# Kernel optimization log

Hardware: AMD Instinct MI355X
Metric: run time of the kernel (lower is better)

Reference implementation:

```python
import jax, jax.numpy as jnp
import numpy as np

N_NODES = 100000
N_HIGH = 20000
N_EDGES = 200000
D = 128
HEADS = 4
EPS = 1e-16


def setup_inputs() -> dict:
    key = jax.random.key(0)
    ks = jax.random.split(key, 9)
    s = 1.0 / np.sqrt(D)
    return {
        "n_features": jax.random.normal(ks[0], (N_NODES, D), jnp.float32),
        "W_src": jax.random.normal(ks[1], (D, HEADS * D), jnp.float32) * s,
        "W_dst": jax.random.normal(ks[2], (D, HEADS * D), jnp.float32) * s,
        "att_src": jax.random.normal(ks[3], (1, HEADS, D), jnp.float32) * s,
        "att_dst": jax.random.normal(ks[4], (1, HEADS, D), jnp.float32) * s,
        "W_high": jax.random.normal(ks[5], (D, D), jnp.float32) * s,
        "b_high": jnp.zeros((D,), jnp.float32),
        "src_idx": jax.random.randint(ks[6], (N_EDGES,), 0, N_NODES),
        "dst_idx": jax.random.randint(ks[7], (N_EDGES,), 0, N_HIGH),
    }


def reference(n_features, W_src, W_dst, att_src, att_dst, W_high, b_high, src_idx, dst_idx):
    # --- edge-wise gather of node features ---
    nn_features = n_features[src_idx]                      # [E, D]
    # --- scatter-mean to hyperedge features, gather back per edge ---
    seg_sum = jax.ops.segment_sum(nn_features, dst_idx, num_segments=N_HIGH)
    cnt = jax.ops.segment_sum(jnp.ones((src_idx.shape[0],), nn_features.dtype), dst_idx, num_segments=N_HIGH)
    h_mean = seg_sum / jnp.maximum(cnt, 1.0)[:, None]       # [H, D]
    h_high_e = h_mean[dst_idx]                              # [E, D]
    # --- per-edge multi-head projections ---
    E = src_idx.shape[0]
    h_node = (nn_features @ W_src).reshape(E, HEADS, D)     # [E, h, D]
    h_high = (h_high_e @ W_dst).reshape(E, HEADS, D)        # [E, h, D]
    # --- attention scores ---
    alpha_src = (h_high * att_src).sum(-1)                  # [E, h]
    alpha_dst = (h_node * att_dst).sum(-1)                  # [E, h]
    alpha = jax.nn.leaky_relu(alpha_src + alpha_dst, 0.2)
    # --- segment softmax over edges grouped by hyperedge id ---
    amax = jax.ops.segment_max(alpha, dst_idx, num_segments=N_HIGH)
    alpha = jnp.exp(alpha - amax[dst_idx])
    asum = jax.ops.segment_sum(alpha, dst_idx, num_segments=N_HIGH)
    alpha = alpha / (asum[dst_idx] + EPS)                   # [E, h]
    # --- weight, head-mean, scatter-sum aggregate ---
    h_node = (h_node * alpha[..., None]).mean(axis=1)       # [E, D]
    h_features = jax.ops.segment_sum(h_node, dst_idx, num_segments=N_HIGH)
    h_features = h_features @ W_high + b_high               # [H, D]
    return (h_features, alpha)
```

## Files before the change

### kernel.cpp

```cpp
#include <hip/hip_runtime.h>
#include <math.h>

#define N_NODES 100000
#define N_HIGH  20000
#define N_EDGES 200000
#define D       128
#define HEADS   4
#define EPSF    1e-16f

typedef __attribute__((ext_vector_type(8))) short bf16x8;
typedef __attribute__((ext_vector_type(4))) float f32x4;
typedef unsigned short ushort_t;
typedef unsigned int uint_t;

__device__ __forceinline__ ushort_t bf16_rn(float f) {
  uint_t u = __float_as_uint(f);
  u = u + 0x7FFFu + ((u >> 16) & 1u);
  return (ushort_t)(u >> 16);
}
__device__ __forceinline__ uint_t pack_bf2(float x, float y) {
  return (uint_t)bf16_rn(x) | ((uint_t)bf16_rn(y) << 16);
}
__device__ __forceinline__ float readlane_f(float v, int q) {
  return __uint_as_float(__builtin_amdgcn_readlane(__float_as_uint(v), q));
}

constexpr size_t OFF_VSRC = 0;
constexpr size_t OFF_VDST = OFF_VSRC + 512 * 4;
constexpr size_t OFF_P    = OFF_VDST + 512 * 4;
constexpr size_t OFF_APK  = OFF_P    + 65536 * 4;
constexpr size_t OFF_CNT  = OFF_APK  + 800000 * 4;
constexpr size_t OFF_OFFS = OFF_CNT  + 20000 * 4;
constexpr size_t OFF_FILL = OFF_OFFS + 20004 * 4;
constexpr size_t OFF_SORT = OFF_FILL + 20000 * 4;
constexpr size_t OFF_G    = OFF_SORT + 200000 * 8;
constexpr size_t OFF_NFB  = OFF_G    + 20000 * 512 * 2;

__global__ __launch_bounds__(256) void k_vp(
    const float* __restrict__ Wsrc, const float* __restrict__ Wdst,
    const float* __restrict__ att_src, const float* __restrict__ att_dst,
    const float* __restrict__ Whigh,
    float* __restrict__ v_src, float* __restrict__ v_dst,
    int* __restrict__ cnt, ushort_t* __restrict__ Pt) {
  __shared__ float red[128];
  if (blockIdx.x < 256) {
    int gid = blockIdx.x * 256 + threadIdx.x;
    if (gid < N_HIGH) cnt[gid] = 0;

    int W = blockIdx.x * 4 + (threadIdx.x >> 6);
    int lane = threadIdx.x & 63;
    int which = W >> 9;
    int idx = W & 511;
    int k = idx >> 2, h = idx & 3;
    const float* wrow = (which ? Wdst : Wsrc) + k * (HEADS * D) + h * D;
    const float* arow = (which ? att_src : att_dst) + h * D;
    float2 wv = ((const float2*)wrow)[lane];
    float2 av = ((const float2*)arow)[lane];
    float s = wv.x * av.x + wv.y * av.y;
#pragma unroll
    for (int o = 32; o; o >>= 1) s += __shfl_xor(s, o);
    if (lane == 0) {
      if (which) v_src[k * HEADS + h] = s;
      else       v_dst[k * HEADS + h] = s;
    }
  } else {
    int hk = blockIdx.x - 256;
    int h = hk >> 7, col = hk & 127;
    int d = threadIdx.x & 127, half = threadIdx.x >> 7;
    const float* ws = Wsrc + col * (HEADS * D) + h * D + half * 64;
    const float* wh = Whigh + (size_t)(half * 64) * D + d;
    float s = 0.f;
#pragma unroll 8
    for (int m = 0; m < 64; ++m) s += ws[m] * wh[(size_t)m * D];
    if (half) red[d] = s;
    __syncthreads();
    if (!half) {
      int kp = (col >> 1) * 8 + h * 2 + (col & 1);
      Pt[(size_t)d * 512 + kp] = bf16_rn(0.25f * (s + red[d]));
    }
  }
}

#define NP_BLOCKS 1563
#define H_BLOCKS  782
__global__ __launch_bounds__(256) void k_nodehist(
    const float* __restrict__ nf,
    const float* __restrict__ v_src, const float* __restrict__ v_dst,
    float4* __restrict__ a_pack,
    const int* __restrict__ dst, int* __restrict__ cnt,
    ushort_t* __restrict__ nfb) {
  __shared__ float nfT[128 * 65];
  __shared__ float4 vsf4[128];
  __shared__ float4 vdf4[128];
  __shared__ float part[8][4][64];
  int t = threadIdx.x;
  if (blockIdx.x >= NP_BLOCKS) {
    int e = (blockIdx.x - NP_BLOCKS) * 256 + t;
    if (e < N_EDGES) atomicAdd(&cnt[dst[e]], 1);
    return;
  }
  int n0 = blockIdx.x * 64;

  if (t < 128) vsf4[t] = ((const float4*)v_src)[t];
  else vdf4[t - 128] = ((const float4*)v_dst)[t - 128];

  const float4* nf4 = (const float4*)nf;
#pragma unroll
  for (int j = 0; j < 8; ++j) {
    int f4 = j * 256 + t;
    int r = f4 >> 5, c4 = f4 & 31;
    int n = n0 + r;
    if (n > N_NODES - 1) n = N_NODES - 1;
    float4 g = nf4[(size_t)n * 32 + c4];
    nfT[(c4 * 4 + 0) * 65 + r] = g.x;
    nfT[(c4 * 4 + 1) * 65 + r] = g.y;
    nfT[(c4 * 4 + 2) * 65 + r] = g.z;
    nfT[(c4 * 4 + 3) * 65 + r] = g.w;
    ushort4 hb;
    hb.x = bf16_rn(g.x); hb.y = bf16_rn(g.y);
    hb.z = bf16_rn(g.z); hb.w = bf16_rn(g.w);
    ((ushort4*)nfb)[(size_t)n * 32 + c4] = hb;
  }
  __syncthreads();

  int l = t & 63, w = t >> 6;
  float as[4] = {0.f, 0.f, 0.f, 0.f};
  float ad[4] = {0.f, 0.f, 0.f, 0.f};
#pragma unroll 8
  for (int kk = 0; kk < 32; ++kk) {
    int k = w * 32 + kk;
    float x = nfT[k * 65 + l];
    float4 s4 = vsf4[k];
    float4 d4 = vdf4[k];
    as[0] += x * s4.x; as[1] += x * s4.y; as[2] += x * s4.z; as[3] += x * s4.w;
    ad[0] += x * d4.x; ad[1] += x * d4.y; ad[2] += x * d4.z; ad[3] += x * d4.w;
  }
#pragma unroll
  for (int v = 0; v < 4; ++v) {
    part[v][w][l] = as[v];
    part[v + 4][w][l] = ad[v];
  }
  __syncthreads();

  if (t < 64) {
    int ll = t;
    if (n0 + ll < N_NODES) {
      float4 o;
      o.x = part[0][0][ll] + part[0][1][ll] + part[0][2][ll] + part[0][3][ll];
      o.y = part[1][0][ll] + part[1][1][ll] + part[1][2][ll] + part[1][3][ll];
      o.z = part[2][0][ll] + part[2][1][ll] + part[2][2][ll] + part[2][3][ll];
      o.w = part[3][0][ll] + part[3][1][ll] + part[3][2][ll] + part[3][3][ll];
      a_pack[(size_t)(n0 + ll) * 2] = o;
    }
  } else if (t < 128) {
    int ll = t - 64;
    if (n0 + ll < N_NODES) {
      float4 o;
      o.x = part[4][0][ll] + part[4][1][ll] + part[4][2][ll] + part[4][3][ll];
      o.y = part[5][0][ll] + part[5][1][ll] + part[5][2][ll] + part[5][3][ll];
      o.z = part[6][0][ll] + part[6][1][ll] + part[6][2][ll] + part[6][3][ll];
      o.w = part[7][0][ll] + part[7][1][ll] + part[7][2][ll] + part[7][3][ll];
      a_pack[(size_t)(n0 + ll) * 2 + 1] = o;
    }
  }
}

#define SCAN_PER 20
__global__ __launch_bounds__(1024) void k_scan(
    const int* __restrict__ cnt, int* __restrict__ offs) {
  __shared__ int sm[1024];
  int t = threadIdx.x;
  int base = t * SCAN_PER;
  int s = 0;
  for (int i = 0; i < SCAN_PER; ++i) {
    int idx = base + i;
    s += (idx < N_HIGH) ? cnt[idx] : 0;
  }
  sm[t] = s;
  __syncthreads();
  for (int o = 1; o < 1024; o <<= 1) {
    int v = (t >= o) ? sm[t - o] : 0;
    __syncthreads();
    if (t >= o) sm[t] += v;
    __syncthreads();
  }
  int run = (t > 0) ? sm[t - 1] : 0;
  for (int i = 0; i < SCAN_PER; ++i) {
    int idx = base + i;
    if (idx < N_HIGH) {
      offs[idx] = run;
      run += cnt[idx];
    }
  }
  if (t == 1023) offs[N_HIGH] = sm[1023];
}

__global__ void k_scatter(const int* __restrict__ dst, const int* __restrict__ src,
                          const int* __restrict__ offs,
                          int* __restrict__ cnt, int2* __restrict__ sorted) {
  int e = blockIdx.x * blockDim.x + threadIdx.x;
  if (e < N_EDGES) {
    int d = dst[e];
    int pos = offs[d] + (atomicSub(&cnt[d], 1) - 1);
    sorted[pos] = make_int2(e, src[e]);
  }
}

#define RS 520
__global__ __launch_bounds__(512) void k_mg(
    const ushort_t* __restrict__ nfb,
    const float4* __restrict__ a_pack,
    const int* __restrict__ offs, const int2* __restrict__ sorted,
    const ushort_t* __restrict__ Pt, const float* __restrict__ b,
    float* __restrict__ alpha_out, float* __restrict__ out) {
  __shared__ ushort_t Gl[16 * RS];
  int t = threadIdx.x;
  int w = t >> 6, lane = t & 63;
  int j0 = blockIdx.x * 16;
  int rowA = w * 2, rowB = rowA + 1;
  int jA = j0 + rowA;
  int oA0 = offs[jA], oA1 = offs[jA + 1], oB1 = offs[jA + 2];
  int oB0 = oA1;
  int degA = oA1 - oA0, degB = oB1 - oB0;

  float2 accA[4], accB[4];
#pragma unroll
  for (int h = 0; h < 4; ++h) {
    accA[h] = make_float2(0.f, 0.f);
    accB[h] = make_float2(0.f, 0.f);
  }

  if (degA <= 64 && degB <= 64) {
    bool actA = lane < degA, actB = lane < degB;
    int idxA = min(oA0 + (actA ? lane : 0), N_EDGES - 1);
    int idxB = min(oB0 + (actB ? lane : 0), N_EDGES - 1);
    int2 esA = sorted[idxA];
    int2 esB = sorted[idxB];
    int eA = esA.x, srA = esA.y;
    int eB = esB.x, srB = esB.y;
    float4 z4 = make_float4(0.f, 0.f, 0.f, 0.f);
    float4 asA = z4, adA = z4, asB = z4, adB = z4;
    if (actA) { asA = a_pack[(size_t)srA * 2]; adA = a_pack[(size_t)srA * 2 + 1]; }
    if (actB) { asB = a_pack[(size_t)srB * 2]; adB = a_pack[(size_t)srB * 2 + 1]; }

    float sA[4] = {asA.x, asA.y, asA.z, asA.w};
    float sB[4] = {asB.x, asB.y, asB.z, asB.w};
#pragma unroll
    for (int o = 32; o; o >>= 1)
#pragma unroll
      for (int h = 0; h < 4; ++h) {
        sA[h] += __shfl_xor(sA[h], o);
        sB[h] += __shfl_xor(sB[h], o);
      }
    float invA = 1.0f / (float)max(degA, 1);
    float invB = 1.0f / (float)max(degB, 1);
    float adv[2][4] = {{adA.x, adA.y, adA.z, adA.w}, {adB.x, adB.y, adB.z, adB.w}};
    float exA[4], exB[4];
#pragma unroll
    for (int h = 0; h < 4; ++h) {
      float pA = sA[h] * invA + adv[0][h];
      float pB = sB[h] * invB + adv[1][h];
      pA = pA >= 0.f ? pA : 0.2f * pA;
      pB = pB >= 0.f ? pB : 0.2f * pB;
      exA[h] = actA ? expf(pA) : 0.f;
      exB[h] = actB ? expf(pB) : 0.f;
    }
    float seA[4] = {exA[0], exA[1], exA[2], exA[3]};
    float seB[4] = {exB[0], exB[1], exB[2], exB[3]};
#pragma unroll
    for (int o = 32; o; o >>= 1)
#pragma unroll
      for (int h = 0; h < 4; ++h) {
        seA[h] += __shfl_xor(seA[h], o);
        seB[h] += __shfl_xor(seB[h], o);
      }
    float alA[4], alB[4];
#pragma unroll
    for (int h = 0; h < 4; ++h) {
      alA[h] = exA[h] / (seA[h] + EPSF);
      alB[h] = exB[h] / (seB[h] + EPSF);
    }
    if (actA)
      ((float4*)alpha_out)[eA] = make_float4(alA[0], alA[1], alA[2], alA[3]);
    if (actB)
      ((float4*)alpha_out)[eB] = make_float4(alB[0], alB[1], alB[2], alB[3]);

    const uint_t* __restrict__ nfbu = (const uint_t*)nfb;
    int dmax = max(degA, degB);
#pragma unroll 8
    for (int q = 0; q < dmax; ++q) {
      int sqA = __builtin_amdgcn_readlane(srA, q);
      int sqB = __builtin_amdgcn_readlane(srB, q);
      uint_t xwA = nfbu[(size_t)sqA * 64 + lane];
      uint_t xwB = nfbu[(size_t)sqB * 64 + lane];
      float a0 = readlane_f(alA[0], q);
      float a1 = readlane_f(alA[1], q);
      float a2 = readlane_f(alA[2], q);
      float a3 = readlane_f(alA[3], q);
      float b0 = readlane_f(alB[0], q);
      float b1 = readlane_f(alB[1], q);
      float b2 = readlane_f(alB[2], q);
      float b3 = readlane_f(alB[3], q);
      float xAx = __uint_as_float(xwA << 16);
      float xAy = __uint_as_float(xwA & 0xFFFF0000u);
      float xBx = __uint_as_float(xwB << 16);
      float xBy = __uint_as_float(xwB & 0xFFFF0000u);
      accA[0].x += a0 * xAx; accA[0].y += a0 * xAy;
      accA[1].x += a1 * xAx; accA[1].y += a1 * xAy;
      accA[2].x += a2 * xAx; accA[2].y += a2 * xAy;
      accA[3].x += a3 * xAx; accA[3].y += a3 * xAy;
      accB[0].x += b0 * xBx; accB[0].y += b0 * xBy;
      accB[1].x += b1 * xBx; accB[1].y += b1 * xBy;
      accB[2].x += b2 * xBx; accB[2].y += b2 * xBy;
      accB[3].x += b3 * xBx; accB[3].y += b3 * xBy;
    }
  } else {
    for (int pick = 0; pick < 2; ++pick) {
      int o0 = pick ? oB0 : oA0;
      int deg = pick ? degB : degA;
      float2* acc = pick ? accB : accA;

      float s[4] = {0.f, 0.f, 0.f, 0.f};
      for (int i = lane; i < deg; i += 64) {
        int2 es = sorted[o0 + i];
        float4 a = a_pack[(size_t)es.y * 2];
        s[0] += a.x; s[1] += a.y; s[2] += a.z; s[3] += a.w;
      }
#pragma unroll
      for (int o = 32; o; o >>= 1)
#pragma unroll
        for (int h = 0; h < 4; ++h) s[h] += __shfl_xor(s[h], o);
      float ah[4];
      float invdeg = 1.0f / (float)max(deg, 1);
#pragma unroll
      for (int h = 0; h < 4; ++h) ah[h] = s[h] * invdeg;

      float se[4] = {0.f, 0.f, 0.f, 0.f};
      for (int i = lane; i < deg; i += 64) {
        int2 es = sorted[o0 + i];
        float4 a = a_pack[(size_t)es.y * 2 + 1];
        float p[4] = {ah[0] + a.x, ah[1] + a.y, ah[2] + a.z, ah[3] + a.w};
#pragma unroll
        for (int h = 0; h < 4; ++h) {
          float pp = p[h] >= 0.f ? p[h] : 0.2f * p[h];
          se[h] += expf(pp);
        }
      }
#pragma unroll
      for (int o = 32; o; o >>= 1)
#pragma unroll
        for (int h = 0; h < 4; ++h) se[h] += __shfl_xor(se[h], o);
      float inv[4];
#pragma unroll
      for (int h = 0; h < 4; ++h) inv[h] = 1.0f / (se[h] + EPSF);

      for (int c0 = 0; c0 < deg; c0 += 64) {
        int i = c0 + lane;
        float al[4] = {0.f, 0.f, 0.f, 0.f};
        int sreg = 0;
        if (i < deg) {
          int2 es = sorted[o0 + i];
          sreg = es.y;
          float4 a = a_pack[(size_t)sreg * 2 + 1];
          float p[4] = {ah[0] + a.x, ah[1] + a.y, ah[2] + a.z, ah[3] + a.w};
#pragma unroll
          for (int h = 0; h < 4; ++h) {
            float pp = p[h] >= 0.f ? p[h] : 0.2f * p[h];
            al[h] = expf(pp) * inv[h];
          }
          ((float4*)alpha_out)[es.x] = make_float4(al[0], al[1], al[2], al[3]);
        }
        int cl = min(64, deg - c0);
#pragma unroll 2
        for (int q = 0; q < cl; ++q) {
          int sq = __builtin_amdgcn_readlane(sreg, q);
          float a0 = readlane_f(al[0], q);
          float a1 = readlane_f(al[1], q);
          float a2 = readlane_f(al[2], q);
          float a3 = readlane_f(al[3], q);
          uint_t xw = ((const uint_t*)nfb)[(size_t)sq * 64 + lane];
          float xx = __uint_as_float(xw << 16);
          float xy = __uint_as_float(xw & 0xFFFF0000u);
          acc[0].x += a0 * xx; acc[0].y += a0 * xy;
          acc[1].x += a1 * xx; acc[1].y += a1 * xy;
          acc[2].x += a2 * xx; acc[2].y += a2 * xy;
          acc[3].x += a3 * xx; acc[3].y += a3 * xy;
        }
      }
    }
  }
  uint4 gwA, gwB;
  gwA.x = pack_bf2(accA[0].x, accA[0].y);
  gwA.y = pack_bf2(accA[1].x, accA[1].y);
  gwA.z = pack_bf2(accA[2].x, accA[2].y);
  gwA.w = pack_bf2(accA[3].x, accA[3].y);
  gwB.x = pack_bf2(accB[0].x, accB[0].y);
  gwB.y = pack_bf2(accB[1].x, accB[1].y);
  gwB.z = pack_bf2(accB[2].x, accB[2].y);
  gwB.w = pack_bf2(accB[3].x, accB[3].y);
  *(uint4*)&Gl[rowA * RS + lane * 8] = gwA;
  *(uint4*)&Gl[rowB * RS + lane * 8] = gwB;
  __syncthreads();

  int lr = lane & 15, lg = lane >> 4;
  f32x4 c0 = (f32x4){0.f, 0.f, 0.f, 0.f};
  const ushort_t* Pa = Pt + (size_t)lr * 512 + lg * 8 + (size_t)w * 16 * 512;
#pragma unroll
  for (int kt = 0; kt < 16; ++kt) {
    bf16x8 a = *(const bf16x8*)&Gl[lr * RS + kt * 32 + lg * 8];
    bf16x8 b0 = *(const bf16x8*)(Pa + kt * 32);
    c0 = __builtin_amdgcn_mfma_f32_16x16x32_bf16(a, b0, c0, 0, 0, 0);
  }
  int col0 = w * 16 + lr;
  float bb0 = b[col0];
#pragma unroll
  for (int r = 0; r < 4; ++r) {
    int row = j0 + lg * 4 + r;
    out[(size_t)row * 128 + col0] = c0[r] + bb0;
  }
}

extern "C" void kernel_launch(void* const* d_in, const int* in_sizes, int n_in,
                              void* d_out, int out_size, void* d_ws, size_t ws_size,
                              hipStream_t stream) {
  const float* nf      = (const float*)d_in[0];
  const float* Wsrc    = (const float*)d_in[1];
  const float* Wdst    = (const float*)d_in[2];
  const float* att_src = (const float*)d_in[3];
  const float* att_dst = (const float*)d_in[4];
  const float* Whigh   = (const float*)d_in[5];
  const float* bhigh   = (const float*)d_in[6];
  const int*   src     = (const int*)d_in[7];
  const int*   dst     = (const int*)d_in[8];

  char* ws = (char*)d_ws;
  float*    v_src  = (float*)(ws + OFF_VSRC);
  float*    v_dst  = (float*)(ws + OFF_VDST);
  ushort_t* Pt     = (ushort_t*)(ws + OFF_P);
  float4*   a_pack = (float4*)(ws + OFF_APK);
  int*      cnt    = (int*)(ws + OFF_CNT);
  int*      offs   = (int*)(ws + OFF_OFFS);
  int2*     sorted = (int2*)(ws + OFF_SORT);
  ushort_t* nfb    = (ushort_t*)(ws + OFF_NFB);

  float* out_h     = (float*)d_out;
  float* out_alpha = (float*)d_out + (size_t)N_HIGH * D;

  k_vp<<<768, 256, 0, stream>>>(Wsrc, Wdst, att_src, att_dst, Whigh,
                                v_src, v_dst, cnt, Pt);
  k_nodehist<<<NP_BLOCKS + H_BLOCKS, 256, 0, stream>>>(
      nf, v_src, v_dst, a_pack, dst, cnt, nfb);
  k_scan<<<1, 1024, 0, stream>>>(cnt, offs);
  k_scatter<<<(N_EDGES + 255) / 256, 256, 0, stream>>>(dst, src, offs, cnt, sorted);
  k_mg<<<N_HIGH / 16, 512, 0, stream>>>(nfb, a_pack, offs, sorted,
                                        Pt, bhigh, out_alpha, out_h);
}
```

Before: 112.7 us.

## Precompute per-hyperedge alpha_src sums via atomics in scatter; warp-shuffle scan

The scatter kernel now gathers each edge's source attention term and adds it atomically into a per-hyperedge float4 sum, so k_mg no longer gathers a_pack source terms and reduces them across the wavefront. The single-block scan is rewritten to use wavefront shuffle prefix sums plus a small shared array of per-wave totals, replacing the many-barrier shared-memory scan, and it keeps the counts in registers instead of reloading them. The trade is four float atomics per edge in scatter and a nondeterministic summation order.

```diff
diff --git a/kernel.cpp b/kernel.cpp
--- a/kernel.cpp
+++ b/kernel.cpp
@@ -35,17 +35,22 @@
 constexpr size_t OFF_SORT = OFF_FILL + 20000 * 4;
 constexpr size_t OFF_G    = OFF_SORT + 200000 * 8;
 constexpr size_t OFF_NFB  = OFF_G    + 20000 * 512 * 2;
+constexpr size_t OFF_AHS  = OFF_NFB  + (size_t)100000 * 128 * 2;
 
 __global__ __launch_bounds__(256) void k_vp(
     const float* __restrict__ Wsrc, const float* __restrict__ Wdst,
     const float* __restrict__ att_src, const float* __restrict__ att_dst,
     const float* __restrict__ Whigh,
     float* __restrict__ v_src, float* __restrict__ v_dst,
-    int* __restrict__ cnt, ushort_t* __restrict__ Pt) {
+    int* __restrict__ cnt, float4* __restrict__ ahsum,
+    ushort_t* __restrict__ Pt) {
   __shared__ float red[128];
   if (blockIdx.x < 256) {
     int gid = blockIdx.x * 256 + threadIdx.x;
-    if (gid < N_HIGH) cnt[gid] = 0;
+    if (gid < N_HIGH) {
+      cnt[gid] = 0;
+      ahsum[gid] = make_float4(0.f, 0.f, 0.f, 0.f);
+    }
 
     int W = blockIdx.x * 4 + (threadIdx.x >> 6);
     int lane = threadIdx.x & 63;
@@ -168,41 +173,56 @@
 #define SCAN_PER 20
 __global__ __launch_bounds__(1024) void k_scan(
     const int* __restrict__ cnt, int* __restrict__ offs) {
-  __shared__ int sm[1024];
+  __shared__ int wsum[16];
   int t = threadIdx.x;
+  int lane = t & 63, wv = t >> 6;
   int base = t * SCAN_PER;
+  int loc[SCAN_PER];
   int s = 0;
+#pragma unroll
   for (int i = 0; i < SCAN_PER; ++i) {
     int idx = base + i;
-    s += (idx < N_HIGH) ? cnt[idx] : 0;
-  }
-  sm[t] = s;
+    loc[i] = (idx < N_HIGH) ? cnt[idx] : 0;
+    s += loc[i];
+  }
+  int tot = s;
+#pragma unroll
+  for (int o = 1; o < 64; o <<= 1) {
+    int v = __shfl_up(tot, o);
+    if (lane >= o) tot += v;
+  }
+  if (lane == 63) wsum[wv] = tot;
   __syncthreads();
-  for (int o = 1; o < 1024; o <<= 1) {
-    int v = (t >= o) ? sm[t - o] : 0;
-    __syncthreads();
-    if (t >= o) sm[t] += v;
-    __syncthreads();
-  }
-  int run = (t > 0) ? sm[t - 1] : 0;
+  int wpre = 0;
+  for (int i = 0; i < 16; ++i) wpre += (i < wv) ? wsum[i] : 0;
+  int run = wpre + tot - s;
+#pragma unroll
   for (int i = 0; i < SCAN_PER; ++i) {
     int idx = base + i;
     if (idx < N_HIGH) {
       offs[idx] = run;
-      run += cnt[idx];
-    }
-  }
-  if (t == 1023) offs[N_HIGH] = sm[1023];
+      run += loc[i];
+    }
+  }
+  if (t == 1023) offs[N_HIGH] = wpre + tot;
 }
 
 __global__ void k_scatter(const int* __restrict__ dst, const int* __restrict__ src,
                           const int* __restrict__ offs,
-                          int* __restrict__ cnt, int2* __restrict__ sorted) {
+                          int* __restrict__ cnt, int2* __restrict__ sorted,
+                          const float4* __restrict__ a_pack,
+                          float* __restrict__ ahsum) {
   int e = blockIdx.x * blockDim.x + threadIdx.x;
   if (e < N_EDGES) {
     int d = dst[e];
+    int sn = src[e];
     int pos = offs[d] + (atomicSub(&cnt[d], 1) - 1);
-    sorted[pos] = make_int2(e, src[e]);
+    sorted[pos] = make_int2(e, sn);
+    float4 a = a_pack[(size_t)sn * 2];
+    atomicAdd(&ahsum[(size_t)d * 4 + 0], a.x);
+    atomicAdd(&ahsum[(size_t)d * 4 + 1], a.y);
+    atomicAdd(&ahsum[(size_t)d * 4 + 2], a.z);
+    atomicAdd(&ahsum[(size_t)d * 4 + 3], a.w);
   }
 }
 
@@ -210,6 +230,7 @@
 __global__ __launch_bounds__(512) void k_mg(
     const ushort_t* __restrict__ nfb,
     const float4* __restrict__ a_pack,
+    const float4* __restrict__ ahsum,
     const int* __restrict__ offs, const int2* __restrict__ sorted,
     const ushort_t* __restrict__ Pt, const float* __restrict__ b,
     float* __restrict__ alpha_out, float* __restrict__ out) {
@@ -239,31 +260,36 @@
     int eA = esA.x, srA = esA.y;
     int eB = esB.x, srB = esB.y;
     float4 z4 = make_float4(0.f, 0.f, 0.f, 0.f);
-    float4 asA = z4, adA = z4, asB = z4, adB = z4;
-    if (actA) { asA = a_pack[(size_t)srA * 2]; adA = a_pack[(size_t)srA * 2 + 1]; }
-    if (actB) { asB = a_pack[(size_t)srB * 2]; adB = a_pack[(size_t)srB * 2 + 1]; }
-
-    float sA[4] = {asA.x, asA.y, asA.z, asA.w};
-    float sB[4] = {asB.x, asB.y, asB.z, asB.w};
-#pragma unroll
-    for (int o = 32; o; o >>= 1)
-#pragma unroll
-      for (int h = 0; h < 4; ++h) {
-        sA[h] += __shfl_xor(sA[h], o);
-        sB[h] += __shfl_xor(sB[h], o);
-      }
+    float4 adA = z4, adB = z4;
+    if (actA) adA = a_pack[(size_t)srA * 2 + 1];
+    if (actB) adB = a_pack[(size_t)srB * 2 + 1];
+    float4 ahA4 = ahsum[jA];
+    float4 ahB4 = ahsum[jA + 1];
     float invA = 1.0f / (float)max(degA, 1);
     float invB = 1.0f / (float)max(degB, 1);
-    float adv[2][4] = {{adA.x, adA.y, adA.z, adA.w}, {adB.x, adB.y, adB.z, adB.w}};
+
     float exA[4], exB[4];
-#pragma unroll
-    for (int h = 0; h < 4; ++h) {
-      float pA = sA[h] * invA + adv[0][h];
-      float pB = sB[h] * invB + adv[1][h];
-      pA = pA >= 0.f ? pA : 0.2f * pA;
-      pB = pB >= 0.f ? pB : 0.2f * pB;
-      exA[h] = actA ? expf(pA) : 0.f;
-      exB[h] = actB ? expf(pB) : 0.f;
+    {
+      float pA0 = ahA4.x * invA + adA.x, pA1 = ahA4.y * invA + adA.y;
+      float pA2 = ahA4.z * invA + adA.z, pA3 = ahA4.w * invA + adA.w;
+      float pB0 = ahB4.x * invB + adB.x, pB1 = ahB4.y * invB + adB.y;
+      float pB2 = ahB4.z * invB + adB.z, pB3 = ahB4.w * invB + adB.w;
+      pA0 = pA0 >= 0.f ? pA0 : 0.2f * pA0;
+      pA1 = pA1 >= 0.f ? pA1 : 0.2f * pA1;
+      pA2 = pA2 >= 0.f ? pA2 : 0.2f * pA2;
+      pA3 = pA3 >= 0.f ? pA3 : 0.2f * pA3;
+      pB0 = pB0 >= 0.f ? pB0 : 0.2f * pB0;
+      pB1 = pB1 >= 0.f ? pB1 : 0.2f * pB1;
+      pB2 = pB2 >= 0.f ? pB2 : 0.2f * pB2;
+      pB3 = pB3 >= 0.f ? pB3 : 0.2f * pB3;
+      exA[0] = actA ? expf(pA0) : 0.f;
+      exA[1] = actA ? expf(pA1) : 0.f;
+      exA[2] = actA ? expf(pA2) : 0.f;
+      exA[3] = actA ? expf(pA3) : 0.f;
+      exB[0] = actB ? expf(pB0) : 0.f;
+      exB[1] = actB ? expf(pB1) : 0.f;
+      exB[2] = actB ? expf(pB2) : 0.f;
+      exB[3] = actB ? expf(pB3) : 0.f;
     }
     float seA[4] = {exA[0], exA[1], exA[2], exA[3]};
     float seB[4] = {exB[0], exB[1], exB[2], exB[3]};
@@ -318,22 +344,12 @@
     for (int pick = 0; pick < 2; ++pick) {
       int o0 = pick ? oB0 : oA0;
       int deg = pick ? degB : degA;
+      int jj = jA + pick;
       float2* acc = pick ? accB : accA;
 
-      float s[4] = {0.f, 0.f, 0.f, 0.f};
-      for (int i = lane; i < deg; i += 64) {
-        int2 es = sorted[o0 + i];
-        float4 a = a_pack[(size_t)es.y * 2];
-        s[0] += a.x; s[1] += a.y; s[2] += a.z; s[3] += a.w;
-      }
-#pragma unroll
-      for (int o = 32; o; o >>= 1)
-#pragma unroll
-        for (int h = 0; h < 4; ++h) s[h] += __shfl_xor(s[h], o);
-      float ah[4];
+      float4 ah4 = ahsum[jj];
       float invdeg = 1.0f / (float)max(deg, 1);
-#pragma unroll
-      for (int h = 0; h < 4; ++h) ah[h] = s[h] * invdeg;
+      float ah[4] = {ah4.x * invdeg, ah4.y * invdeg, ah4.z * invdeg, ah4.w * invdeg};
 
       float se[4] = {0.f, 0.f, 0.f, 0.f};
       for (int i = lane; i < deg; i += 64) {
@@ -442,16 +458,18 @@
   int*      offs   = (int*)(ws + OFF_OFFS);
   int2*     sorted = (int2*)(ws + OFF_SORT);
   ushort_t* nfb    = (ushort_t*)(ws + OFF_NFB);
+  float4*   ahsum  = (float4*)(ws + OFF_AHS);
 
   float* out_h     = (float*)d_out;
   float* out_alpha = (float*)d_out + (size_t)N_HIGH * D;
 
   k_vp<<<768, 256, 0, stream>>>(Wsrc, Wdst, att_src, att_dst, Whigh,
-                                v_src, v_dst, cnt, Pt);
+                                v_src, v_dst, cnt, ahsum, Pt);
   k_nodehist<<<NP_BLOCKS + H_BLOCKS, 256, 0, stream>>>(
       nf, v_src, v_dst, a_pack, dst, cnt, nfb);
   k_scan<<<1, 1024, 0, stream>>>(cnt, offs);
-  k_scatter<<<(N_EDGES + 255) / 256, 256, 0, stream>>>(dst, src, offs, cnt, sorted);
-  k_mg<<<N_HIGH / 16, 512, 0, stream>>>(nfb, a_pack, offs, sorted,
+  k_scatter<<<(N_EDGES + 255) / 256, 256, 0, stream>>>(
+      dst, src, offs, cnt, sorted, a_pack, (float*)ahsum);
+  k_mg<<<N_HIGH / 16, 512, 0, stream>>>(nfb, a_pack, ahsum, offs, sorted,
                                         Pt, bhigh, out_alpha, out_h);
 }
```

New measurement: 143.8 us. +27.6%, slower.
